# Performance work log

Measured on AMD Instinct MI355X. Metric: run time of the kernel, lower is better.

The kernel has to match this reference:

```python
import jax, jax.numpy as jnp
import numpy as np

EPS = 1e-5   # torch.nn.BatchNorm default eps
K = 27       # 3x3x3 octree conv kernel size


def _octree_conv(x, neigh, W):
    """Octree sparse 3x3x3 conv: per kernel offset, gather neighbor features
    and matmul. x: [N, C], neigh: [N, K] int32, W: [K, C, D] -> [N, D].
    Loop over the 27 fixed offsets avoids materializing the [N, 27, C] gather."""
    out = jnp.zeros((x.shape[0], W.shape[2]), dtype=x.dtype)
    for k in range(K):
        out = out + x[neigh[:, k]] @ W[k]
    return out


def _bn(x, gamma, beta):
    # BatchNorm1d in training mode: normalize over the node dimension.
    m = jnp.mean(x, axis=0)
    v = jnp.var(x, axis=0)
    return (x - m) * jax.lax.rsqrt(v + EPS) * gamma + beta


def setup_inputs() -> dict:
    key = jax.random.key(0)
    ks = jax.random.split(key, 5)
    N, Cin, Cout = 500000, 128, 256  # bottleneck=1 => channelb == Cout
    data = jax.random.normal(ks[0], (N, Cin), dtype=jnp.float32)
    neigh = jax.random.randint(ks[1], (N, K), 0, N, dtype=jnp.int32)
    Wa = jax.random.normal(ks[2], (K, Cin, Cout), dtype=jnp.float32) / np.sqrt(K * Cin)
    Wb = jax.random.normal(ks[3], (K, Cout, Cout), dtype=jnp.float32) / np.sqrt(K * Cout)
    W1 = jax.random.normal(ks[4], (Cin, Cout), dtype=jnp.float32) / np.sqrt(Cin)
    return {
        "data": data, "neigh": neigh, "depth": 5,
        "Wa": Wa, "ga": jnp.ones(Cout), "ba": jnp.zeros(Cout),
        "Wb": Wb, "gb": jnp.ones(Cout), "bb": jnp.zeros(Cout),
        "W1": W1, "gs": jnp.ones(Cout), "bs": jnp.zeros(Cout),
    }


def reference(data, neigh, depth, Wa, ga, ba, Wb, gb, bb, W1, gs, bs):
    # stride == 1 => no maxpool, depth unchanged (depth unused beyond routing).
    conv1 = jax.nn.relu(_bn(_octree_conv(data, neigh, Wa), ga, ba))  # Conv3x3+BN+ReLU
    conv2 = _bn(_octree_conv(conv1, neigh, Wb), gb, bb)              # Conv3x3+BN
    shortcut = _bn(data @ W1, gs, bs)                                # Conv1x1+BN (Cin != Cout)
    return jax.nn.relu(conv2 + shortcut)
```

## Files before the change

### kernel.cpp

```cpp
#include <hip/hip_runtime.h>
#include <hip/hip_bf16.h>
#include <stdint.h>

typedef __attribute__((ext_vector_type(8))) short bf16x8;
typedef __attribute__((ext_vector_type(4))) float f32x4;

#define AS1(p) ((const __attribute__((address_space(1))) void*)(p))
#define AS3(p) ((__attribute__((address_space(3))) void*)(p))

__device__ __forceinline__ unsigned short f2bf(float f) {
    union { float f; unsigned u; } v; v.f = f;
    unsigned r = v.u + 0x7fffu + ((v.u >> 16) & 1u);
    return (unsigned short)(r >> 16);
}
__device__ __forceinline__ float bf2f(unsigned short h) {
    union { unsigned u; float f; } v; v.u = ((unsigned)h) << 16;
    return v.f;
}

template<int CIN, bool GATHER, bool OUT_BF16>
__global__ __launch_bounds__(512, 2) void conv_kernel(
    const unsigned short* __restrict__ in,
    const int* __restrict__ neigh,
    const unsigned short* __restrict__ Wt,
    void* __restrict__ outp,
    float* __restrict__ stats,
    int N, int NK)
{
    constexpr int KT = 64;
    constexpr int NKT = CIN / KT;
    __shared__ unsigned short Alds[2][128 * KT];
    __shared__ unsigned short Blds[2][256 * KT];
    __shared__ int nlds[GATHER ? 128 * 27 : 8];

    const int tid  = threadIdx.x;
    const int lane = tid & 63;
    const int wid  = tid >> 6;
    const int wr   = wid >> 2, wc = wid & 3;
    const int brow = blockIdx.x * 128;

    if (GATHER) {
        for (int s = tid; s < 128 * 27; s += 512) {
            int r = s / 27, kk = s - r * 27;
            int grow = brow + r;
            nlds[s] = (grow < N) ? neigh[(size_t)grow * 27 + kk] : 0;
        }
        __syncthreads();
    }

    const int T = NK * NKT;

    auto stage = [&](int t) {
        const int k = t / NKT, kt = t - (t / NKT) * NKT;
        const int b = t & 1;
        #pragma unroll
        for (int i = 0; i < 2; ++i) {
            int s = i * 512 + tid;
            int r = s >> 3, seg = s & 7;
            int g = GATHER ? nlds[r * 27 + k] : (brow + r);
            const char* src = (const char*)in + ((size_t)g * CIN + kt * KT) * 2
                            + ((seg ^ (r & 7)) * 16);
            __builtin_amdgcn_global_load_lds(AS1(src),
                AS3((char*)&Alds[b][0] + (i * 512 + wid * 64) * 16), 16, 0, 0);
        }
        #pragma unroll
        for (int i = 0; i < 4; ++i) {
            int s = i * 512 + tid;
            int c = s >> 3, seg = s & 7;
            const char* src = (const char*)Wt
                + (((size_t)k * 256 + c) * CIN + kt * KT) * 2
                + ((seg ^ (c & 7)) * 16);
            __builtin_amdgcn_global_load_lds(AS1(src),
                AS3((char*)&Blds[b][0] + (i * 512 + wid * 64) * 16), 16, 0, 0);
        }
    };

    f32x4 acc[4][4] = {};

    stage(0);
    for (int t = 0; t < T; ++t) {
        if (t + 1 < T) {
            stage(t + 1);
            __builtin_amdgcn_sched_barrier(0);
            asm volatile("s_waitcnt vmcnt(6)" ::: "memory");
        } else {
            __builtin_amdgcn_sched_barrier(0);
            asm volatile("s_waitcnt vmcnt(0)" ::: "memory");
        }
        __builtin_amdgcn_sched_barrier(0);
        __builtin_amdgcn_s_barrier();
        __builtin_amdgcn_sched_barrier(0);

        const char* Ab = (const char*)&Alds[t & 1][0];
        const char* Bb = (const char*)&Blds[t & 1][0];
        bf16x8 bfr[4][2];
        #pragma unroll
        for (int n = 0; n < 4; ++n)
            #pragma unroll
            for (int kk = 0; kk < 2; ++kk) {
                int c = wc * 64 + n * 16 + (lane & 15);
                int byte = (c * 128 + kk * 64 + ((lane >> 4) * 16)) ^ ((c & 7) << 4);
                bfr[n][kk] = *(const bf16x8*)(Bb + byte);
            }
        #pragma unroll
        for (int m = 0; m < 4; ++m) {
            bf16x8 af[2];
            #pragma unroll
            for (int kk = 0; kk < 2; ++kk) {
                int r = wr * 64 + m * 16 + (lane & 15);
                int byte = (r * 128 + kk * 64 + ((lane >> 4) * 16)) ^ ((r & 7) << 4);
                af[kk] = *(const bf16x8*)(Ab + byte);
            }
            #pragma unroll
            for (int n = 0; n < 4; ++n) {
                acc[m][n] = __builtin_amdgcn_mfma_f32_16x16x32_bf16(af[0], bfr[n][0], acc[m][n], 0, 0, 0);
                acc[m][n] = __builtin_amdgcn_mfma_f32_16x16x32_bf16(af[1], bfr[n][1], acc[m][n], 0, 0, 0);
            }
        }
        __builtin_amdgcn_sched_barrier(0);
        __builtin_amdgcn_s_barrier();
        __builtin_amdgcn_sched_barrier(0);
    }

    #pragma unroll
    for (int n = 0; n < 4; ++n) {
        float s = 0.f, q = 0.f;
        #pragma unroll
        for (int m = 0; m < 4; ++m)
            #pragma unroll
            for (int j = 0; j < 4; ++j) {
                int row = brow + wr * 64 + m * 16 + ((lane >> 4) * 4) + j;
                float v = (row < N) ? acc[m][n][j] : 0.f;
                s += v; q += v * v;
            }
        s += __shfl_xor(s, 16); s += __shfl_xor(s, 32);
        q += __shfl_xor(q, 16); q += __shfl_xor(q, 32);
        if (lane < 16) {
            int col = wc * 64 + n * 16 + lane;
            atomicAdd(&stats[col], s);
            atomicAdd(&stats[256 + col], q);
        }
    }
    #pragma unroll
    for (int m = 0; m < 4; ++m) {
        #pragma unroll
        for (int j = 0; j < 4; ++j) {
            int row = brow + wr * 64 + m * 16 + ((lane >> 4) * 4) + j;
            if (row < N) {
                #pragma unroll
                for (int n = 0; n < 4; ++n) {
                    int col = wc * 64 + n * 16 + (lane & 15);
                    float v = acc[m][n][j];
                    if (OUT_BF16)
                        ((unsigned short*)outp)[(size_t)row * 256 + col] = f2bf(v);
                    else
                        __builtin_nontemporal_store(v, &((float*)outp)[(size_t)row * 256 + col]);
                }
            }
        }
    }
}

__global__ void cast_x_kernel(const float* __restrict__ x, unsigned short* __restrict__ xb, size_t n8) {
    size_t stride = (size_t)gridDim.x * blockDim.x;
    for (size_t i = (size_t)blockIdx.x * blockDim.x + threadIdx.x; i < n8; i += stride) {
        const float4* p = (const float4*)(x + i * 8);
        float4 f0 = p[0], f1 = p[1];
        unsigned short o[8];
        o[0] = f2bf(f0.x); o[1] = f2bf(f0.y); o[2] = f2bf(f0.z); o[3] = f2bf(f0.w);
        o[4] = f2bf(f1.x); o[5] = f2bf(f1.y); o[6] = f2bf(f1.z); o[7] = f2bf(f1.w);
        *(uint4*)(xb + i * 8) = *(uint4*)o;
    }
}

__global__ void cast_wT_kernel(const float* __restrict__ w, unsigned short* __restrict__ wt,
                               int NK, int CI, int CO) {
    int total = NK * CI * CO;
    int stride = gridDim.x * blockDim.x;
    for (int id = blockIdx.x * blockDim.x + threadIdx.x; id < total; id += stride) {
        int ci = id % CI;
        int t  = id / CI;
        int co = t % CO;
        int k  = t / CO;
        wt[id] = f2bf(w[((size_t)k * CI + ci) * CO + co]);
    }
}

__global__ void finalize_kernel(const float* __restrict__ stats, const float* __restrict__ gamma,
                                const float* __restrict__ beta, float* __restrict__ coef, float invN) {
    int c = threadIdx.x;
    float mean = stats[c] * invN;
    float var  = fmaxf(stats[256 + c] * invN - mean * mean, 0.f);
    float a = gamma[c] * rsqrtf(var + 1e-5f);
    coef[c] = a;
    coef[256 + c] = beta[c] - mean * a;
}

__global__ void bn_relu_kernel(unsigned short* __restrict__ buf, const float* __restrict__ coef, size_t n8) {
    size_t stride = (size_t)gridDim.x * blockDim.x;
    for (size_t i = (size_t)blockIdx.x * blockDim.x + threadIdx.x; i < n8; i += stride) {
        uint4 v = *(uint4*)(buf + i * 8);
        unsigned short* h = (unsigned short*)&v;
        int cb = (int)((i * 8) & 255);
        #pragma unroll
        for (int j = 0; j < 8; ++j) {
            float f = bf2f(h[j]) * coef[cb + j] + coef[256 + cb + j];
            h[j] = f2bf(fmaxf(f, 0.f));
        }
        *(uint4*)(buf + i * 8) = v;
    }
}

__global__ void final_kernel(float* __restrict__ out, const unsigned short* __restrict__ sc,
                             const float* __restrict__ c2, const float* __restrict__ cs, size_t n4) {
    size_t stride = (size_t)gridDim.x * blockDim.x;
    for (size_t i = (size_t)blockIdx.x * blockDim.x + threadIdx.x; i < n4; i += stride) {
        float4 o = *(float4*)(out + i * 4);
        ushort4 s4 = *(const ushort4*)(sc + i * 4);
        int cb = (int)((i * 4) & 255);
        float r;
        r = o.x * c2[cb + 0] + c2[256 + cb + 0] + bf2f(s4.x) * cs[cb + 0] + cs[256 + cb + 0]; o.x = fmaxf(r, 0.f);
        r = o.y * c2[cb + 1] + c2[256 + cb + 1] + bf2f(s4.y) * cs[cb + 1] + cs[256 + cb + 1]; o.y = fmaxf(r, 0.f);
        r = o.z * c2[cb + 2] + c2[256 + cb + 2] + bf2f(s4.z) * cs[cb + 2] + cs[256 + cb + 2]; o.z = fmaxf(r, 0.f);
        r = o.w * c2[cb + 3] + c2[256 + cb + 3] + bf2f(s4.w) * cs[cb + 3] + cs[256 + cb + 3]; o.w = fmaxf(r, 0.f);
        *(float4*)(out + i * 4) = o;
    }
}

extern "C" void kernel_launch(void* const* d_in, const int* in_sizes, int n_in,
                              void* d_out, int out_size, void* d_ws, size_t ws_size,
                              hipStream_t stream) {
    const float* data = (const float*)d_in[0];
    const int*   neigh = (const int*)d_in[1];
    const float* Wa = (const float*)d_in[3];
    const float* ga = (const float*)d_in[4];
    const float* ba = (const float*)d_in[5];
    const float* Wb = (const float*)d_in[6];
    const float* gb = (const float*)d_in[7];
    const float* bb = (const float*)d_in[8];
    const float* W1 = (const float*)d_in[9];
    const float* gs = (const float*)d_in[10];
    const float* bs = (const float*)d_in[11];

    const int N = in_sizes[0] / 128;
    const int nblk = (N + 127) / 128;
    const int Npad = nblk * 128;

    char* ws = (char*)d_ws;
    float* stats1 = (float*)(ws + 0);
    float* stats2 = (float*)(ws + 2048);
    float* statss = (float*)(ws + 4096);
    float* c1     = (float*)(ws + 6144);
    float* c2     = (float*)(ws + 8192);
    float* cs     = (float*)(ws + 10240);
    unsigned short* WaT = (unsigned short*)(ws + 16384);
    unsigned short* WbT = WaT + (size_t)27 * 256 * 128;
    unsigned short* W1T = WbT + (size_t)27 * 256 * 256;
    unsigned short* Xb  = W1T + (size_t)256 * 128;
    unsigned short* buf1 = Xb + (size_t)Npad * 128;

    hipMemsetAsync(d_ws, 0, 16384, stream);
    if (Npad > N)
        hipMemsetAsync(Xb + (size_t)N * 128, 0, (size_t)(Npad - N) * 128 * 2, stream);

    cast_x_kernel<<<2048, 256, 0, stream>>>(data, Xb, (size_t)N * 128 / 8);
    cast_wT_kernel<<<1024, 256, 0, stream>>>(Wa, WaT, 27, 128, 256);
    cast_wT_kernel<<<1024, 256, 0, stream>>>(Wb, WbT, 27, 256, 256);
    cast_wT_kernel<<<64, 256, 0, stream>>>(W1, W1T, 1, 128, 256);

    conv_kernel<128, true, true><<<nblk, 512, 0, stream>>>(Xb, neigh, WaT, buf1, stats1, N, 27);
    finalize_kernel<<<1, 256, 0, stream>>>(stats1, ga, ba, c1, 1.0f / N);
    bn_relu_kernel<<<2048, 256, 0, stream>>>(buf1, c1, (size_t)N * 256 / 8);
    conv_kernel<256, true, false><<<nblk, 512, 0, stream>>>(buf1, neigh, WbT, d_out, stats2, N, 27);
    conv_kernel<128, false, true><<<nblk, 512, 0, stream>>>(Xb, nullptr, W1T, buf1, statss, N, 1);
    finalize_kernel<<<1, 256, 0, stream>>>(stats2, gb, bb, c2, 1.0f / N);
    finalize_kernel<<<1, 256, 0, stream>>>(statss, gs, bs, cs, 1.0f / N);
    final_kernel<<<2048, 256, 0, stream>>>((float*)d_out, buf1, c2, cs, (size_t)N * 256 / 4);
}
```

Before: 4.675 ms.

## Load MFMA fragments directly from global memory into registers, dropping LDS staging

Replaces the double-buffered LDS staging (global_load_lds plus workgroup barriers) with per-wave loads of A and B fragments straight into registers. Two register fragment sets alternate so the next step's loads overlap the current MFMAs. This removes LDS round-trips and block-wide barriers. In exchange, each wave now fetches its own copy of data that was previously shared through LDS, so global/L2 traffic goes up. The two fragment sets also raise register pressure under the 512x2 launch bounds, with a risk of spills.

```diff
diff --git a/kernel.cpp b/kernel.cpp
--- a/kernel.cpp
+++ b/kernel.cpp
@@ -4,9 +4,6 @@
 
 typedef __attribute__((ext_vector_type(8))) short bf16x8;
 typedef __attribute__((ext_vector_type(4))) float f32x4;
-
-#define AS1(p) ((const __attribute__((address_space(1))) void*)(p))
-#define AS3(p) ((__attribute__((address_space(3))) void*)(p))
 
 __device__ __forceinline__ unsigned short f2bf(float f) {
     union { float f; unsigned u; } v; v.f = f;
@@ -27,10 +24,7 @@
     float* __restrict__ stats,
     int N, int NK)
 {
-    constexpr int KT = 64;
-    constexpr int NKT = CIN / KT;
-    __shared__ unsigned short Alds[2][128 * KT];
-    __shared__ unsigned short Blds[2][256 * KT];
+    constexpr int NKT = CIN / 64;
     __shared__ int nlds[GATHER ? 128 * 27 : 8];
 
     const int tid  = threadIdx.x;
@@ -48,78 +42,71 @@
         __syncthreads();
     }
 
-    const int T = NK * NKT;
-
-    auto stage = [&](int t) {
-        const int k = t / NKT, kt = t - (t / NKT) * NKT;
-        const int b = t & 1;
-        #pragma unroll
-        for (int i = 0; i < 2; ++i) {
-            int s = i * 512 + tid;
-            int r = s >> 3, seg = s & 7;
-            int g = GATHER ? nlds[r * 27 + k] : (brow + r);
-            const char* src = (const char*)in + ((size_t)g * CIN + kt * KT) * 2
-                            + ((seg ^ (r & 7)) * 16);
-            __builtin_amdgcn_global_load_lds(AS1(src),
-                AS3((char*)&Alds[b][0] + (i * 512 + wid * 64) * 16), 16, 0, 0);
-        }
-        #pragma unroll
-        for (int i = 0; i < 4; ++i) {
-            int s = i * 512 + tid;
-            int c = s >> 3, seg = s & 7;
-            const char* src = (const char*)Wt
-                + (((size_t)k * 256 + c) * CIN + kt * KT) * 2
-                + ((seg ^ (c & 7)) * 16);
-            __builtin_amdgcn_global_load_lds(AS1(src),
-                AS3((char*)&Blds[b][0] + (i * 512 + wid * 64) * 16), 16, 0, 0);
-        }
+    const int rbase = wr * 64 + (lane & 15);
+    const int chunk = (lane >> 4) * 16;
+
+    int boff[4];
+    #pragma unroll
+    for (int n = 0; n < 4; ++n)
+        boff[n] = (wc * 64 + n * 16 + (lane & 15)) * CIN * 2 + chunk;
+
+    struct Frag { bf16x8 a[4][2]; bf16x8 b[4][2]; };
+
+    f32x4 acc[4][4] = {};
+    Frag F0, F1;
+    int idc[4], idn[4];
+
+    auto loadidx = [&](int k, int* id) {
+        #pragma unroll
+        for (int m = 0; m < 4; ++m)
+            id[m] = GATHER ? nlds[(rbase + m * 16) * 27 + k] : (brow + rbase + m * 16);
     };
-
-    f32x4 acc[4][4] = {};
-
-    stage(0);
-    for (int t = 0; t < T; ++t) {
-        if (t + 1 < T) {
-            stage(t + 1);
-            __builtin_amdgcn_sched_barrier(0);
-            asm volatile("s_waitcnt vmcnt(6)" ::: "memory");
-        } else {
-            __builtin_amdgcn_sched_barrier(0);
-            asm volatile("s_waitcnt vmcnt(0)" ::: "memory");
-        }
-        __builtin_amdgcn_sched_barrier(0);
-        __builtin_amdgcn_s_barrier();
-        __builtin_amdgcn_sched_barrier(0);
-
-        const char* Ab = (const char*)&Alds[t & 1][0];
-        const char* Bb = (const char*)&Blds[t & 1][0];
-        bf16x8 bfr[4][2];
-        #pragma unroll
-        for (int n = 0; n < 4; ++n)
-            #pragma unroll
-            for (int kk = 0; kk < 2; ++kk) {
-                int c = wc * 64 + n * 16 + (lane & 15);
-                int byte = (c * 128 + kk * 64 + ((lane >> 4) * 16)) ^ ((c & 7) << 4);
-                bfr[n][kk] = *(const bf16x8*)(Bb + byte);
-            }
+    auto loadfrag = [&](Frag& F, const int* id, int k, int kt) {
+        const char* wb = (const char*)Wt + ((size_t)k * 256 * CIN) * 2 + kt * 128;
+        #pragma unroll
+        for (int n = 0; n < 4; ++n) {
+            F.b[n][0] = *(const bf16x8*)(wb + boff[n]);
+            F.b[n][1] = *(const bf16x8*)(wb + boff[n] + 64);
+        }
         #pragma unroll
         for (int m = 0; m < 4; ++m) {
-            bf16x8 af[2];
-            #pragma unroll
-            for (int kk = 0; kk < 2; ++kk) {
-                int r = wr * 64 + m * 16 + (lane & 15);
-                int byte = (r * 128 + kk * 64 + ((lane >> 4) * 16)) ^ ((r & 7) << 4);
-                af[kk] = *(const bf16x8*)(Ab + byte);
-            }
+            const char* ab = (const char*)in + ((size_t)id[m] * CIN) * 2 + kt * 128 + chunk;
+            F.a[m][0] = *(const bf16x8*)(ab);
+            F.a[m][1] = *(const bf16x8*)(ab + 64);
+        }
+    };
+    auto domfma = [&](Frag& F) {
+        #pragma unroll
+        for (int m = 0; m < 4; ++m)
             #pragma unroll
             for (int n = 0; n < 4; ++n) {
-                acc[m][n] = __builtin_amdgcn_mfma_f32_16x16x32_bf16(af[0], bfr[n][0], acc[m][n], 0, 0, 0);
-                acc[m][n] = __builtin_amdgcn_mfma_f32_16x16x32_bf16(af[1], bfr[n][1], acc[m][n], 0, 0, 0);
-            }
-        }
-        __builtin_amdgcn_sched_barrier(0);
-        __builtin_amdgcn_s_barrier();
-        __builtin_amdgcn_sched_barrier(0);
+                acc[m][n] = __builtin_amdgcn_mfma_f32_16x16x32_bf16(F.a[m][0], F.b[n][0], acc[m][n], 0, 0, 0);
+                acc[m][n] = __builtin_amdgcn_mfma_f32_16x16x32_bf16(F.a[m][1], F.b[n][1], acc[m][n], 0, 0, 0);
+            }
+    };
+
+    loadidx(0, idc);
+    loadfrag(F0, idc, 0, 0);
+
+    for (int k = 0; k < NK; ++k) {
+        if (GATHER && k + 1 < NK) loadidx(k + 1, idn);
+        #pragma unroll
+        for (int kt = 0; kt < NKT; ++kt) {
+            if ((kt & 1) == 0) {
+                if (kt + 1 < NKT)      loadfrag(F1, idc, k, kt + 1);
+                else if (k + 1 < NK)   loadfrag(F1, idn, k + 1, 0);
+                domfma(F0);
+            } else {
+                if (kt + 1 < NKT)      loadfrag(F0, idc, k, kt + 1);
+                else if (k + 1 < NK)   loadfrag(F0, idn, k + 1, 0);
+                domfma(F1);
+            }
+        }
+        if (GATHER) {
+            #pragma unroll
+            for (int m = 0; m < 4; ++m) idc[m] = idn[m];
+        } else {
+        }
     }
 
     #pragma unroll
```

New measurement: 9.911 ms. 112% more time.

## Triple-buffer gathered A tiles to prefetch two stages ahead, raise MFMA priority

Applied to the files above, without the earlier changes.

Splits tile staging into separate A (gathered activations) and B (weights) loaders. A gets a third LDS buffer so neighbor-gathered rows are fetched two K-steps ahead while weights stay double-buffered, with the vmcnt waits adjusted to match. The aim is to hide the long latency of the random row gathers behind more MFMA work. It also wraps the MFMA bursts in s_setprio to favor the math wave. The cost is an extra 16KB of LDS and more in-flight loads, which could hurt occupancy.

```diff
diff --git a/kernel.cpp b/kernel.cpp
--- a/kernel.cpp
+++ b/kernel.cpp
@@ -29,7 +29,7 @@
 {
     constexpr int KT = 64;
     constexpr int NKT = CIN / KT;
-    __shared__ unsigned short Alds[2][128 * KT];
+    __shared__ unsigned short Alds[3][128 * KT];
     __shared__ unsigned short Blds[2][256 * KT];
     __shared__ int nlds[GATHER ? 128 * 27 : 8];
 
@@ -50,9 +50,9 @@
 
     const int T = NK * NKT;
 
-    auto stage = [&](int t) {
+    auto stageA = [&](int t) {
         const int k = t / NKT, kt = t - (t / NKT) * NKT;
-        const int b = t & 1;
+        char* dst = (char*)&Alds[t % 3][0];
         #pragma unroll
         for (int i = 0; i < 2; ++i) {
             int s = i * 512 + tid;
@@ -61,8 +61,12 @@
             const char* src = (const char*)in + ((size_t)g * CIN + kt * KT) * 2
                             + ((seg ^ (r & 7)) * 16);
             __builtin_amdgcn_global_load_lds(AS1(src),
-                AS3((char*)&Alds[b][0] + (i * 512 + wid * 64) * 16), 16, 0, 0);
-        }
+                AS3(dst + (i * 512 + wid * 64) * 16), 16, 0, 0);
+        }
+    };
+    auto stageB = [&](int t) {
+        const int k = t / NKT, kt = t - (t / NKT) * NKT;
+        char* dst = (char*)&Blds[t & 1][0];
         #pragma unroll
         for (int i = 0; i < 4; ++i) {
             int s = i * 512 + tid;
@@ -71,27 +75,28 @@
                 + (((size_t)k * 256 + c) * CIN + kt * KT) * 2
                 + ((seg ^ (c & 7)) * 16);
             __builtin_amdgcn_global_load_lds(AS1(src),
-                AS3((char*)&Blds[b][0] + (i * 512 + wid * 64) * 16), 16, 0, 0);
+                AS3(dst + (i * 512 + wid * 64) * 16), 16, 0, 0);
         }
     };
 
     f32x4 acc[4][4] = {};
 
-    stage(0);
+    stageA(0);
+    stageB(0);
+    if (T > 1) stageA(1);
+
     for (int t = 0; t < T; ++t) {
-        if (t + 1 < T) {
-            stage(t + 1);
-            __builtin_amdgcn_sched_barrier(0);
-            asm volatile("s_waitcnt vmcnt(6)" ::: "memory");
-        } else {
-            __builtin_amdgcn_sched_barrier(0);
-            asm volatile("s_waitcnt vmcnt(0)" ::: "memory");
-        }
+        if (t + 1 < T) stageB(t + 1);
+        if (t + 2 < T) stageA(t + 2);
+        __builtin_amdgcn_sched_barrier(0);
+        if (t + 2 < T)      asm volatile("s_waitcnt vmcnt(8)" ::: "memory");
+        else if (t + 1 < T) asm volatile("s_waitcnt vmcnt(6)" ::: "memory");
+        else                asm volatile("s_waitcnt vmcnt(0)" ::: "memory");
         __builtin_amdgcn_sched_barrier(0);
         __builtin_amdgcn_s_barrier();
         __builtin_amdgcn_sched_barrier(0);
 
-        const char* Ab = (const char*)&Alds[t & 1][0];
+        const char* Ab = (const char*)&Alds[t % 3][0];
         const char* Bb = (const char*)&Blds[t & 1][0];
         bf16x8 bfr[4][2];
         #pragma unroll
@@ -111,11 +116,13 @@
                 int byte = (r * 128 + kk * 64 + ((lane >> 4) * 16)) ^ ((r & 7) << 4);
                 af[kk] = *(const bf16x8*)(Ab + byte);
             }
+            __builtin_amdgcn_s_setprio(1);
             #pragma unroll
             for (int n = 0; n < 4; ++n) {
                 acc[m][n] = __builtin_amdgcn_mfma_f32_16x16x32_bf16(af[0], bfr[n][0], acc[m][n], 0, 0, 0);
                 acc[m][n] = __builtin_amdgcn_mfma_f32_16x16x32_bf16(af[1], bfr[n][1], acc[m][n], 0, 0, 0);
             }
+            __builtin_amdgcn_s_setprio(0);
         }
         __builtin_amdgcn_sched_barrier(0);
         __builtin_amdgcn_s_barrier();
```

After: 4.747 ms. Within noise of the previous version (+1.5%).
